# Performance work log

Hardware: AMD Instinct MI355X
Metric: run time of the kernel (lower is better)

Reference implementation:

```python
import jax, jax.numpy as jnp
import numpy as np

B, CIN, H, W = 64, 3, 96, 96
COUT, KH, KW = 96, 5, 5
STRIDE, PAD = 2, 2
LR, K_TOP, DELTA, P_LEB = 0.02, 2, -0.4, 3.0
PREC = 1e-30


def im2col(x):
    # torch nn.Unfold ordering: channel-major (C, kh, kw) flattened -> [B, C*KH*KW, L]
    xp = jnp.pad(x, ((0, 0), (0, 0), (PAD, PAD), (PAD, PAD)))
    Hout = (H + 2 * PAD - KH) // STRIDE + 1
    Wout = (W + 2 * PAD - KW) // STRIDE + 1
    cols = []
    for i in range(KH):  # small fixed kernel loop (25 slices)
        for j in range(KW):
            cols.append(xp[:, :, i:i + STRIDE * (Hout - 1) + 1:STRIDE,
                           j:j + STRIDE * (Wout - 1) + 1:STRIDE])
    patches = jnp.stack(cols, axis=2)  # [B, C, KH*KW, Hout, Wout]
    return patches.reshape(x.shape[0], CIN * KH * KW, Hout * Wout)  # [B, K, L]


def setup_inputs() -> dict:
    key = jax.random.key(0)
    k1, k2 = jax.random.split(key)
    inp = jax.random.normal(k1, (B, CIN, H, W), dtype=jnp.float32)
    weight = jax.random.normal(k2, (COUT, CIN, KH, KW), dtype=jnp.float32)  # init.normal_
    return {"input": inp, "weight": weight}


def reference(input, weight):
    # standard conv forward (F.conv2d, no bias)
    out = jax.lax.conv_general_dilated(
        input, weight, (STRIDE, STRIDE), [(PAD, PAD), (PAD, PAD)],
        dimension_numbers=("NCHW", "OIHW", "NCHW"))

    # --- Krotov-Hopfield Hebbian update ---
    pre = im2col(input)                      # [B, K, L]
    Wm = weight.reshape(COUT, -1)            # [O, K]
    # sign(W) * |W|^(p-1) @ pre
    tot = jnp.einsum("ok,bkl->bol", jnp.sign(Wm) * jnp.abs(Wm) ** (P_LEB - 1.0), pre)  # [B,O,L]

    Bn, _, L = tot.shape
    _, idx = jax.lax.top_k(tot.transpose(0, 2, 1), K_TOP)   # [B, L, k] over output channels
    vals = jnp.concatenate([jnp.ones((1,), tot.dtype),
                            jnp.full((K_TOP - 1,), DELTA, tot.dtype)])  # top-1 -> 1.0, rest -> delta
    act = jnp.zeros((Bn, L, COUT), tot.dtype).at[
        jnp.arange(Bn)[:, None, None], jnp.arange(L)[None, :, None], idx
    ].set(jnp.broadcast_to(vals, (Bn, L, K_TOP)))
    act = act.transpose(0, 2, 1)             # [B, O, L]

    yx = jnp.einsum("bol,bkl->ok", act, pre) / L          # mean over L, sum over batch
    yy = (act * tot).sum(0).mean(1)                        # [O]
    ds = yx - yy[:, None] * Wm                             # [O, K]
    nc = jnp.maximum(jnp.max(jnp.abs(ds)), PREC)
    new_weight = weight + LR * (ds / nc).reshape(weight.shape)
    return out, new_weight
```

## Files before the change

kernel.cpp:

```cpp
#include <hip/hip_runtime.h>

#define B_     64
#define HW_    96
#define COUT_  96
#define KK_    75
#define KP_    76
#define KPAD   96
#define HOUT_  48
#define L_     2304
#define LR_    0.02f
#define DELTA_ -0.4f
#define OUT_ELEMS (B_*COUT_*L_)
#define CL2    256
#define NPART  (B_*9)
#define ROW    (COUT_*KK_ + COUT_)
#define XPITCH 100
#define XSLOTS 3368
#define X2ROWS 15
#define X2N    4500

typedef __attribute__((ext_vector_type(8))) short short8v;
typedef __attribute__((ext_vector_type(4))) float float4v;
typedef __attribute__((ext_vector_type(4))) unsigned uint4v;

__device__ __forceinline__ unsigned short f2bf(float f) {
  unsigned u = __float_as_uint(f);
  u += 0x7fff + ((u >> 16) & 1);
  return (unsigned short)(u >> 16);
}

__device__ __forceinline__ void ins2(float v, int o, float& v1, int& o1,
                                     float& v2, int& o2) {
  bool b1 = (v > v1) || (v == v1 && o < o1);
  bool b2 = (v > v2) || (v == v2 && o < o2);
  if (b1)      { v2 = v1; o2 = o1; v1 = v; o1 = o; }
  else if (b2) { v2 = v;  o2 = o; }
}

__global__ __launch_bounds__(256) void k0_prep(const float* __restrict__ w,
                                               unsigned short* __restrict__ wbf) {
  int i = blockIdx.x * 256 + threadIdx.x;
  if (i >= 192 * KPAD) return;
  int row = i / KPAD, k = i - row * KPAD;
  float v = 0.0f;
  if (k < KK_) {
    float ww = w[(row % COUT_) * KK_ + k];
    v = (row < COUT_) ? ww : ww * fabsf(ww);
  }
  wbf[i] = f2bf(v);
}

__device__ __forceinline__ int wswz(int blk, int row) {
  return (blk < 8) ? (blk ^ (row & 7)) : (blk ^ (row & 3));
}

__global__ __launch_bounds__(256, 3) void k1_mfma(
    const float* __restrict__ x, const unsigned short* __restrict__ wbf,
    float* __restrict__ out, float4* __restrict__ top2)
{
  __shared__ __align__(16) unsigned short wlds[192 * KPAD];
  __shared__ __align__(16) float xs[XSLOTS];
  const int tid = threadIdx.x;
  const int lane = tid & 63, wq = tid >> 6;
  const int b = blockIdx.y;
  const int bx = blockIdx.x;
  const int col = lane & 15, g = lane >> 4;
  const float* xb = x + (size_t)b * (3 * HW_ * HW_);

  #pragma unroll
  for (int i = 0; i < 9; ++i) {
    int id = tid + i * 256;
    int row = id / 12, blk = id - row * 12;
    uint4v v = *(const uint4v*)(wbf + row * KPAD + blk * 8);
    *(uint4v*)((char*)wlds + row * 192 + wswz(blk, row) * 16) = v;
  }

  const int ihbase = 8 * bx - 2;
  #pragma unroll
  for (int i = 0; i < 14; ++i) {
    int idx = tid + i * 256;
    if (idx < XSLOTS) {
      int row = idx / XPITCH, iwr = idx - row * XPITCH;
      int c = row / 11, ihr = row - c * 11;
      int ih = ihbase + ihr, iw = iwr - 2;
      float v = 0.0f;
      if (c < 3 && (unsigned)ih < (unsigned)HW_ && (unsigned)iw < (unsigned)HW_)
        v = xb[(c * HW_ + ih) * HW_ + iw];
      xs[idx] = v;
    }
  }

  int offs[12][2];
  {
    const int base_fl = wq * 200 + 2 * col;
    #pragma unroll
    for (int kt = 0; kt < 3; ++kt)
      #pragma unroll
      for (int e2 = 0; e2 < 4; ++e2)
        #pragma unroll
        for (int par = 0; par < 2; ++par) {
          int k = kt * 32 + g * 8 + 2 * e2 + par;
          int c = k / 25, r = k - 25 * c, ki = r / 5, kj = r - 5 * ki;
          int fl = (k < KK_) ? base_fl + (c * 11 + ki) * XPITCH + kj
                             : 33 * XPITCH;
          offs[kt * 4 + e2][par] = fl * 4;
        }
  }

  __syncthreads();

  short8v bfr[3][3];
  #pragma unroll
  for (int nt = 0; nt < 3; ++nt)
    #pragma unroll
    for (int kt = 0; kt < 3; ++kt) {
      uint4v pk;
      #pragma unroll
      for (int e2 = 0; e2 < 4; ++e2) {
        const float* p0 = (const float*)((const char*)xs + offs[kt*4+e2][0]);
        const float* p1 = (const float*)((const char*)xs + offs[kt*4+e2][1]);
        float v0 = p0[nt * 32];
        float v1 = p1[nt * 32];
        pk[e2] = (unsigned)f2bf(v0) | ((unsigned)f2bf(v1) << 16);
      }
      bfr[nt][kt] = __builtin_bit_cast(short8v, pk);
    }

  const int lrow0 = (4 * bx + wq) * 48;
  float4v acc[3][6];

  #pragma unroll
  for (int nt = 0; nt < 3; ++nt)
    #pragma unroll
    for (int mt = 0; mt < 6; ++mt) acc[nt][mt] = (float4v)(0.0f);
  #pragma unroll
  for (int kt = 0; kt < 3; ++kt) {
    const int blk = kt * 4 + g;
    #pragma unroll
    for (int mt = 0; mt < 6; ++mt) {
      const int row = mt * 16 + col;
      short8v afr = *(const short8v*)(
          (const char*)wlds + row * 192 + wswz(blk, row) * 16);
      #pragma unroll
      for (int nt = 0; nt < 3; ++nt)
        acc[nt][mt] = __builtin_amdgcn_mfma_f32_16x16x32_bf16(
            afr, bfr[nt][kt], acc[nt][mt], 0, 0, 0);
    }
  }
  #pragma unroll
  for (int mt = 0; mt < 6; ++mt)
    #pragma unroll
    for (int r = 0; r < 4; ++r) {
      const int ch = mt * 16 + g * 4 + r;
      float* op = out + ((size_t)b * COUT_ + ch) * L_ + lrow0 + col;
      #pragma unroll
      for (int nt = 0; nt < 3; ++nt) op[nt * 16] = acc[nt][mt][r];
    }

  #pragma unroll
  for (int nt = 0; nt < 3; ++nt)
    #pragma unroll
    for (int mt = 0; mt < 6; ++mt) acc[nt][mt] = (float4v)(0.0f);
  #pragma unroll
  for (int kt = 0; kt < 3; ++kt) {
    const int blk = kt * 4 + g;
    #pragma unroll
    for (int mt = 0; mt < 6; ++mt) {
      const int row = 96 + mt * 16 + col;
      short8v afr = *(const short8v*)(
          (const char*)wlds + row * 192 + wswz(blk, row) * 16);
      #pragma unroll
      for (int nt = 0; nt < 3; ++nt)
        acc[nt][mt] = __builtin_amdgcn_mfma_f32_16x16x32_bf16(
            afr, bfr[nt][kt], acc[nt][mt], 0, 0, 0);
    }
  }
  #pragma unroll
  for (int nt = 0; nt < 3; ++nt) {
    float v1 = -3.0e38f, v2 = -3.0e38f;
    int o1 = 0x7fffffff, o2 = 0x7fffffff;
    #pragma unroll
    for (int mt = 0; mt < 6; ++mt)
      #pragma unroll
      for (int r = 0; r < 4; ++r)
        ins2(acc[nt][mt][r], mt * 16 + g * 4 + r, v1, o1, v2, o2);
    #pragma unroll
    for (int st = 0; st < 2; ++st) {
      const int d = (st == 0) ? 16 : 32;
      float bv1 = __shfl_xor(v1, d, 64);
      int   bo1 = __shfl_xor(o1, d, 64);
      float bv2 = __shfl_xor(v2, d, 64);
      int   bo2 = __shfl_xor(o2, d, 64);
      ins2(bv1, bo1, v1, o1, v2, o2);
      ins2(bv2, bo2, v1, o1, v2, o2);
    }
    if (g == 0)
      top2[(size_t)b * L_ + lrow0 + nt * 16 + col] =
          make_float4(v1, __int_as_float(o1), v2, __int_as_float(o2));
  }
}

__global__ __launch_bounds__(256, 1) void k2_gemm(
    const float* __restrict__ x, const float4* __restrict__ top2,
    float* __restrict__ part)
{
  __shared__ __align__(16) unsigned short actS[COUT_ * CL2];
  __shared__ __align__(16) unsigned short preT[COUT_ * CL2];
  __shared__ __align__(16) float xs2[X2N];
  __shared__ float yyS[COUT_];
  const int tid = threadIdx.x;
  const int b = blockIdx.y;
  const int pos = tid;
  const float* xb = x + (size_t)b * (3 * HW_ * HW_);

  {
    float4* a4 = (float4*)actS;
    float4* p4 = (float4*)preT;
    #pragma unroll
    for (int i = 0; i < 12; ++i) {
      a4[tid + i * 256] = make_float4(0, 0, 0, 0);
      p4[tid + i * 256] = make_float4(0, 0, 0, 0);
    }
    if (tid < COUT_) yyS[tid] = 0.0f;
  }

  const int l0 = blockIdx.x * CL2;
  const int oh0 = l0 / HOUT_;
  const int ihb2 = 2 * oh0 - 2;
  #pragma unroll
  for (int i = 0; i < 18; ++i) {
    int idx = tid + i * 256;
    if (idx < X2N) {
      int row = idx / XPITCH, iwr = idx - row * XPITCH;
      int c = row / X2ROWS, ihr = row - c * X2ROWS;
      int ih = ihb2 + ihr, iw = iwr - 2;
      float v = 0.0f;
      if ((unsigned)ih < (unsigned)HW_ && (unsigned)iw < (unsigned)HW_)
        v = xb[(c * HW_ + ih) * HW_ + iw];
      xs2[idx] = v;
    }
  }
  __syncthreads();

  {
    float pre[KK_];
    const int dl = l0 + pos;
    const int oh = dl / HOUT_, ow = dl - oh * HOUT_;
    const float* xl = xs2 + (2 * (oh - oh0)) * XPITCH + 2 * ow;
    #pragma unroll
    for (int c = 0; c < 3; ++c)
      #pragma unroll
      for (int ki = 0; ki < 5; ++ki)
        #pragma unroll
        for (int kj = 0; kj < 5; ++kj)
          pre[c * 25 + ki * 5 + kj] = xl[(c * X2ROWS + ki) * XPITCH + kj];

    const int pblk = pos >> 3, plo = (pos & 7) << 1;
    #pragma unroll
    for (int k = 0; k < KK_; ++k) {
      int byteoff = k * 512 + ((pblk ^ (k & 7)) << 4) + plo;
      *(unsigned short*)((char*)preT + byteoff) = f2bf(pre[k]);
    }
    float4 t2 = top2[(size_t)b * L_ + dl];
    int o1 = __float_as_int(t2.y), o2 = __float_as_int(t2.w);
    *(unsigned short*)((char*)actS + o1 * 512 + ((pblk ^ (o1 & 7)) << 4) + plo)
        = 0x3F80;
    *(unsigned short*)((char*)actS + o2 * 512 + ((pblk ^ (o2 & 7)) << 4) + plo)
        = f2bf(DELTA_);
    atomicAdd(&yyS[o1], t2.x);
    atomicAdd(&yyS[o2], DELTA_ * t2.z);
  }
  __syncthreads();

  const int lane = tid & 63, w = tid >> 6;
  const int col = lane & 15, g = lane >> 4;
  const int mb = (w >> 1) * 48, nb = (w & 1) * 48;

  float4v acc[3][3];
  #pragma unroll
  for (int mt = 0; mt < 3; ++mt)
    #pragma unroll
    for (int nt = 0; nt < 3; ++nt) acc[mt][nt] = (float4v)(0.0f);

  #pragma unroll
  for (int kt = 0; kt < 8; ++kt) {
    short8v a[3], bf[3];
    #pragma unroll
    for (int mt = 0; mt < 3; ++mt) {
      int row = mb + mt * 16 + col;
      a[mt] = *(const short8v*)((char*)actS + row * 512 +
                                (((kt * 4 + g) ^ (row & 7)) << 4));
    }
    #pragma unroll
    for (int nt = 0; nt < 3; ++nt) {
      int row = nb + nt * 16 + col;
      bf[nt] = *(const short8v*)((char*)preT + row * 512 +
                                 (((kt * 4 + g) ^ (row & 7)) << 4));
    }
    #pragma unroll
    for (int mt = 0; mt < 3; ++mt)
      #pragma unroll
      for (int nt = 0; nt < 3; ++nt)
        acc[mt][nt] = __builtin_amdgcn_mfma_f32_16x16x32_bf16(
            a[mt], bf[nt], acc[mt][nt], 0, 0, 0);
  }
  __syncthreads();

  float* prow = part + (size_t)(b * 9 + blockIdx.x) * ROW;
  #pragma unroll
  for (int mt = 0; mt < 3; ++mt)
    #pragma unroll
    for (int nt = 0; nt < 3; ++nt)
      #pragma unroll
      for (int r = 0; r < 4; ++r) {
        int m = mb + mt * 16 + g * 4 + r;
        int n = nb + nt * 16 + col;
        if (n < KK_) prow[m * KK_ + n] = acc[mt][nt][r];
      }
  if (tid < COUT_) prow[COUT_ * KK_ + tid] = yyS[tid];
}

__global__ __launch_bounds__(256) void k3_reduce(
    const float* __restrict__ part, float* __restrict__ finals)
{
  __shared__ float red[4][64];
  const int e = blockIdx.x * 64 + (threadIdx.x & 63);
  const int seg = threadIdx.x >> 6;
  float s = 0.0f;
  for (int p = seg * (NPART / 4); p < (seg + 1) * (NPART / 4); ++p)
    s += part[(size_t)p * ROW + e];
  red[seg][threadIdx.x & 63] = s;
  __syncthreads();
  if (seg == 0) {
    int ll = threadIdx.x & 63;
    finals[e] = (red[0][ll] + red[1][ll]) + (red[2][ll] + red[3][ll]);
  }
}

__global__ __launch_bounds__(256) void k4_finalize(
    const float* __restrict__ w, const float* __restrict__ finals,
    float* __restrict__ outw)
{
  __shared__ float dsS[COUT_ * KK_];
  __shared__ float wmax[4];
  __shared__ float ncS;
  const int tid = threadIdx.x;
  float m = 0.0f;
  for (int i = tid; i < COUT_ * KK_; i += 256) {
    int o = i / KK_;
    float d = finals[i] - finals[COUT_ * KK_ + o] * w[i];
    dsS[i] = d;
    m = fmaxf(m, fabsf(d));
  }
  #pragma unroll
  for (int s = 32; s > 0; s >>= 1) m = fmaxf(m, __shfl_xor(m, s, 64));
  if ((tid & 63) == 0) wmax[tid >> 6] = m;
  __syncthreads();
  if (tid == 0) {
    float n = fmaxf(fmaxf(wmax[0], wmax[1]), fmaxf(wmax[2], wmax[3]));
    ncS = fmaxf(n, 1e-30f);
  }
  __syncthreads();
  const float scale = LR_ / ncS;
  for (int i = tid; i < COUT_ * KK_; i += 256) {
    outw[i] = w[i] + scale * dsS[i];
  }
}

extern "C" void kernel_launch(void* const* d_in, const int* in_sizes, int n_in,
                              void* d_out, int out_size, void* d_ws, size_t ws_size,
                              hipStream_t stream) {
  (void)in_sizes; (void)n_in; (void)out_size; (void)ws_size;
  const float* x = (const float*)d_in[0];
  const float* w = (const float*)d_in[1];
  float* out  = (float*)d_out;
  float* outw = out + OUT_ELEMS;

  unsigned short* wbf = (unsigned short*)d_ws;
  float4* top2 = (float4*)((char*)d_ws + 192 * KPAD * 2);
  float*  part = (float*)((char*)top2 + (size_t)B_ * L_ * sizeof(float4));
  float*  finals = part + (size_t)NPART * ROW;

  k0_prep   <<<dim3((192 * KPAD + 255) / 256), 256, 0, stream>>>(w, wbf);
  k1_mfma   <<<dim3(12, B_), 256, 0, stream>>>(x, wbf, out, top2);
  k2_gemm   <<<dim3(9, B_), 256, 0, stream>>>(x, top2, part);
  k3_reduce <<<dim3(ROW / 64), 256, 0, stream>>>(part, finals);
  k4_finalize<<<dim3(1), 256, 0, stream>>>(w, finals, outw);
}
```

Before: 122.7 us.

## Drop LDS weight staging in conv kernel and shrink Hebbian GEMM tiles

```diff
diff --git a/kernel.cpp b/kernel.cpp
--- a/kernel.cpp
+++ b/kernel.cpp
@@ -4,20 +4,19 @@
 #define HW_    96
 #define COUT_  96
 #define KK_    75
-#define KP_    76
 #define KPAD   96
 #define HOUT_  48
 #define L_     2304
 #define LR_    0.02f
 #define DELTA_ -0.4f
 #define OUT_ELEMS (B_*COUT_*L_)
-#define CL2    256
-#define NPART  (B_*9)
-#define ROW    (COUT_*KK_ + COUT_)
 #define XPITCH 100
 #define XSLOTS 3368
-#define X2ROWS 15
-#define X2N    4500
+#define C2     192
+#define NPART  (B_*12)
+#define ROW    (COUT_*KK_ + COUT_)
+#define X2P    99
+#define X2N    (33*X2P)
 
 typedef __attribute__((ext_vector_type(8))) short short8v;
 typedef __attribute__((ext_vector_type(4))) float float4v;
@@ -50,15 +49,10 @@
   wbf[i] = f2bf(v);
 }
 
-__device__ __forceinline__ int wswz(int blk, int row) {
-  return (blk < 8) ? (blk ^ (row & 7)) : (blk ^ (row & 3));
-}
-
-__global__ __launch_bounds__(256, 3) void k1_mfma(
+__global__ __launch_bounds__(256, 4) void k1_mfma(
     const float* __restrict__ x, const unsigned short* __restrict__ wbf,
     float* __restrict__ out, float4* __restrict__ top2)
 {
-  __shared__ __align__(16) unsigned short wlds[192 * KPAD];
   __shared__ __align__(16) float xs[XSLOTS];
   const int tid = threadIdx.x;
   const int lane = tid & 63, wq = tid >> 6;
@@ -66,14 +60,6 @@
   const int bx = blockIdx.x;
   const int col = lane & 15, g = lane >> 4;
   const float* xb = x + (size_t)b * (3 * HW_ * HW_);
-
-  #pragma unroll
-  for (int i = 0; i < 9; ++i) {
-    int id = tid + i * 256;
-    int row = id / 12, blk = id - row * 12;
-    uint4v v = *(const uint4v*)(wbf + row * KPAD + blk * 8);
-    *(uint4v*)((char*)wlds + row * 192 + wswz(blk, row) * 16) = v;
-  }
 
   const int ihbase = 8 * bx - 2;
   #pragma unroll
@@ -109,9 +95,11 @@
 
   __syncthreads();
 
-  short8v bfr[3][3];
-  #pragma unroll
-  for (int nt = 0; nt < 3; ++nt)
+  const int lrow0 = (4 * bx + wq) * 48;
+
+  #pragma unroll 1
+  for (int nt = 0; nt < 3; ++nt) {
+    short8v bfr[3];
     #pragma unroll
     for (int kt = 0; kt < 3; ++kt) {
       uint4v pk;
@@ -123,67 +111,45 @@
         float v1 = p1[nt * 32];
         pk[e2] = (unsigned)f2bf(v0) | ((unsigned)f2bf(v1) << 16);
       }
-      bfr[nt][kt] = __builtin_bit_cast(short8v, pk);
-    }
-
-  const int lrow0 = (4 * bx + wq) * 48;
-  float4v acc[3][6];
-
-  #pragma unroll
-  for (int nt = 0; nt < 3; ++nt)
-    #pragma unroll
-    for (int mt = 0; mt < 6; ++mt) acc[nt][mt] = (float4v)(0.0f);
-  #pragma unroll
-  for (int kt = 0; kt < 3; ++kt) {
-    const int blk = kt * 4 + g;
+      bfr[kt] = __builtin_bit_cast(short8v, pk);
+    }
+
+    float4v accW[6], accT[6];
     #pragma unroll
     for (int mt = 0; mt < 6; ++mt) {
-      const int row = mt * 16 + col;
-      short8v afr = *(const short8v*)(
-          (const char*)wlds + row * 192 + wswz(blk, row) * 16);
-      #pragma unroll
-      for (int nt = 0; nt < 3; ++nt)
-        acc[nt][mt] = __builtin_amdgcn_mfma_f32_16x16x32_bf16(
-            afr, bfr[nt][kt], acc[nt][mt], 0, 0, 0);
-    }
-  }
-  #pragma unroll
-  for (int mt = 0; mt < 6; ++mt)
-    #pragma unroll
-    for (int r = 0; r < 4; ++r) {
-      const int ch = mt * 16 + g * 4 + r;
-      float* op = out + ((size_t)b * COUT_ + ch) * L_ + lrow0 + col;
-      #pragma unroll
-      for (int nt = 0; nt < 3; ++nt) op[nt * 16] = acc[nt][mt][r];
-    }
-
-  #pragma unroll
-  for (int nt = 0; nt < 3; ++nt)
-    #pragma unroll
-    for (int mt = 0; mt < 6; ++mt) acc[nt][mt] = (float4v)(0.0f);
-  #pragma unroll
-  for (int kt = 0; kt < 3; ++kt) {
-    const int blk = kt * 4 + g;
-    #pragma unroll
-    for (int mt = 0; mt < 6; ++mt) {
-      const int row = 96 + mt * 16 + col;
-      short8v afr = *(const short8v*)(
-          (const char*)wlds + row * 192 + wswz(blk, row) * 16);
-      #pragma unroll
-      for (int nt = 0; nt < 3; ++nt)
-        acc[nt][mt] = __builtin_amdgcn_mfma_f32_16x16x32_bf16(
-            afr, bfr[nt][kt], acc[nt][mt], 0, 0, 0);
-    }
-  }
-  #pragma unroll
-  for (int nt = 0; nt < 3; ++nt) {
+      accW[mt] = (float4v)(0.0f);
+      accT[mt] = (float4v)(0.0f);
+    }
+    #pragma unroll
+    for (int kt = 0; kt < 3; ++kt) {
+      #pragma unroll
+      for (int mt = 0; mt < 6; ++mt) {
+        short8v aW = *(const short8v*)(
+            wbf + (mt * 16 + col) * KPAD + kt * 32 + g * 8);
+        accW[mt] = __builtin_amdgcn_mfma_f32_16x16x32_bf16(
+            aW, bfr[kt], accW[mt], 0, 0, 0);
+        short8v aT = *(const short8v*)(
+            wbf + (96 + mt * 16 + col) * KPAD + kt * 32 + g * 8);
+        accT[mt] = __builtin_amdgcn_mfma_f32_16x16x32_bf16(
+            aT, bfr[kt], accT[mt], 0, 0, 0);
+      }
+    }
+
+    #pragma unroll
+    for (int mt = 0; mt < 6; ++mt)
+      #pragma unroll
+      for (int r = 0; r < 4; ++r) {
+        const int ch = mt * 16 + g * 4 + r;
+        out[((size_t)b * COUT_ + ch) * L_ + lrow0 + nt * 16 + col] = accW[mt][r];
+      }
+
     float v1 = -3.0e38f, v2 = -3.0e38f;
     int o1 = 0x7fffffff, o2 = 0x7fffffff;
     #pragma unroll
     for (int mt = 0; mt < 6; ++mt)
       #pragma unroll
       for (int r = 0; r < 4; ++r)
-        ins2(acc[nt][mt][r], mt * 16 + g * 4 + r, v1, o1, v2, o2);
+        ins2(accT[mt][r], mt * 16 + g * 4 + r, v1, o1, v2, o2);
     #pragma unroll
     for (int st = 0; st < 2; ++st) {
       const int d = (st == 0) ? 16 : 32;
@@ -200,73 +166,70 @@
   }
 }
 
-__global__ __launch_bounds__(256, 1) void k2_gemm(
+__global__ __launch_bounds__(256, 2) void k2_gemm(
     const float* __restrict__ x, const float4* __restrict__ top2,
     float* __restrict__ part)
 {
-  __shared__ __align__(16) unsigned short actS[COUT_ * CL2];
-  __shared__ __align__(16) unsigned short preT[COUT_ * CL2];
-  __shared__ __align__(16) float xs2[X2N];
+  __shared__ __align__(16) unsigned short actS[COUT_ * C2];
+  __shared__ __align__(16) unsigned short preT[COUT_ * C2];
+  __shared__ __align__(16) unsigned short xsb[X2N + 13];
   __shared__ float yyS[COUT_];
   const int tid = threadIdx.x;
   const int b = blockIdx.y;
-  const int pos = tid;
+  const int bx = blockIdx.x;
+  const int l0 = bx * C2;
   const float* xb = x + (size_t)b * (3 * HW_ * HW_);
 
   {
     float4* a4 = (float4*)actS;
-    float4* p4 = (float4*)preT;
-    #pragma unroll
-    for (int i = 0; i < 12; ++i) {
-      a4[tid + i * 256] = make_float4(0, 0, 0, 0);
-      p4[tid + i * 256] = make_float4(0, 0, 0, 0);
+    #pragma unroll
+    for (int i = 0; i < 9; ++i) a4[tid + i * 256] = make_float4(0, 0, 0, 0);
+    float4* p4 = (float4*)((char*)preT + KK_ * (C2 * 2));
+    if (tid < 252) {
+      p4[2 * tid]     = make_float4(0, 0, 0, 0);
+      p4[2 * tid + 1] = make_float4(0, 0, 0, 0);
     }
     if (tid < COUT_) yyS[tid] = 0.0f;
   }
 
-  const int l0 = blockIdx.x * CL2;
-  const int oh0 = l0 / HOUT_;
-  const int ihb2 = 2 * oh0 - 2;
-  #pragma unroll
-  for (int i = 0; i < 18; ++i) {
+  const int ihb2 = 8 * bx - 2;
+  #pragma unroll
+  for (int i = 0; i < 13; ++i) {
     int idx = tid + i * 256;
     if (idx < X2N) {
-      int row = idx / XPITCH, iwr = idx - row * XPITCH;
-      int c = row / X2ROWS, ihr = row - c * X2ROWS;
+      int row = idx / X2P, iwr = idx - row * X2P;
+      int c = row / 11, ihr = row - c * 11;
       int ih = ihb2 + ihr, iw = iwr - 2;
       float v = 0.0f;
-      if ((unsigned)ih < (unsigned)HW_ && (unsigned)iw < (unsigned)HW_)
+      if (c < 3 && (unsigned)ih < (unsigned)HW_ && (unsigned)iw < (unsigned)HW_)
         v = xb[(c * HW_ + ih) * HW_ + iw];
-      xs2[idx] = v;
-    }
-  }
-  __syncthreads();
-
-  {
-    float pre[KK_];
-    const int dl = l0 + pos;
-    const int oh = dl / HOUT_, ow = dl - oh * HOUT_;
-    const float* xl = xs2 + (2 * (oh - oh0)) * XPITCH + 2 * ow;
+      xsb[idx] = f2bf(v);
+    }
+  }
+  __syncthreads();
+
+  if (tid < C2) {
+    const int pos = tid;
+    const int ohr = pos / HOUT_, ow = pos - ohr * HOUT_;
+    const int pblk = pos >> 3, plo = (pos & 7) << 1;
+    const unsigned short* xl = xsb + (2 * ohr) * X2P + 2 * ow;
     #pragma unroll
     for (int c = 0; c < 3; ++c)
       #pragma unroll
       for (int ki = 0; ki < 5; ++ki)
         #pragma unroll
-        for (int kj = 0; kj < 5; ++kj)
-          pre[c * 25 + ki * 5 + kj] = xl[(c * X2ROWS + ki) * XPITCH + kj];
-
-    const int pblk = pos >> 3, plo = (pos & 7) << 1;
-    #pragma unroll
-    for (int k = 0; k < KK_; ++k) {
-      int byteoff = k * 512 + ((pblk ^ (k & 7)) << 4) + plo;
-      *(unsigned short*)((char*)preT + byteoff) = f2bf(pre[k]);
-    }
-    float4 t2 = top2[(size_t)b * L_ + dl];
+        for (int kj = 0; kj < 5; ++kj) {
+          int k = c * 25 + ki * 5 + kj;
+          unsigned short v = xl[(c * 11 + ki) * X2P + kj];
+          *(unsigned short*)((char*)preT +
+              k * (C2 * 2) + ((pblk ^ (k & 7)) << 4) + plo) = v;
+        }
+    float4 t2 = top2[(size_t)b * L_ + l0 + pos];
     int o1 = __float_as_int(t2.y), o2 = __float_as_int(t2.w);
-    *(unsigned short*)((char*)actS + o1 * 512 + ((pblk ^ (o1 & 7)) << 4) + plo)
-        = 0x3F80;
-    *(unsigned short*)((char*)actS + o2 * 512 + ((pblk ^ (o2 & 7)) << 4) + plo)
-        = f2bf(DELTA_);
+    *(unsigned short*)((char*)actS +
+        o1 * (C2 * 2) + ((pblk ^ (o1 & 7)) << 4) + plo) = 0x3F80;
+    *(unsigned short*)((char*)actS +
+        o2 * (C2 * 2) + ((pblk ^ (o2 & 7)) << 4) + plo) = f2bf(DELTA_);
     atomicAdd(&yyS[o1], t2.x);
     atomicAdd(&yyS[o2], DELTA_ * t2.z);
   }
@@ -283,18 +246,18 @@
     for (int nt = 0; nt < 3; ++nt) acc[mt][nt] = (float4v)(0.0f);
 
   #pragma unroll
-  for (int kt = 0; kt < 8; ++kt) {
+  for (int kt = 0; kt < 6; ++kt) {
     short8v a[3], bf[3];
     #pragma unroll
     for (int mt = 0; mt < 3; ++mt) {
       int row = mb + mt * 16 + col;
-      a[mt] = *(const short8v*)((char*)actS + row * 512 +
+      a[mt] = *(const short8v*)((char*)actS + row * (C2 * 2) +
                                 (((kt * 4 + g) ^ (row & 7)) << 4));
     }
     #pragma unroll
     for (int nt = 0; nt < 3; ++nt) {
       int row = nb + nt * 16 + col;
-      bf[nt] = *(const short8v*)((char*)preT + row * 512 +
+      bf[nt] = *(const short8v*)((char*)preT + row * (C2 * 2) +
                                  (((kt * 4 + g) ^ (row & 7)) << 4));
     }
     #pragma unroll
@@ -306,7 +269,7 @@
   }
   __syncthreads();
 
-  float* prow = part + (size_t)(b * 9 + blockIdx.x) * ROW;
+  float* prow = part + (size_t)(b * 12 + bx) * ROW;
   #pragma unroll
   for (int mt = 0; mt < 3; ++mt)
     #pragma unroll
@@ -383,7 +346,7 @@
 
   k0_prep   <<<dim3((192 * KPAD + 255) / 256), 256, 0, stream>>>(w, wbf);
   k1_mfma   <<<dim3(12, B_), 256, 0, stream>>>(x, wbf, out, top2);
-  k2_gemm   <<<dim3(9, B_), 256, 0, stream>>>(x, top2, part);
+  k2_gemm   <<<dim3(12, B_), 256, 0, stream>>>(x, top2, part);
   k3_reduce <<<dim3(ROW / 64), 256, 0, stream>>>(part, finals);
   k4_finalize<<<dim3(1), 256, 0, stream>>>(w, finals, outw);
 }
```

Result: slower. 171.7 us (+40.0%).
